# Kernel optimization log

Hardware: AMD Instinct MI355X
Metric: run time of the kernel (lower is better)

## Reference

```python
import jax, jax.numpy as jnp
import numpy as np

B, C, N = 16, 64, 2048
K, KS, OC = 20, 20, 64
BN_EPS = 1e-5


def setup_inputs() -> dict:
    key = jax.random.key(0)
    k1, k2, k3, k4 = jax.random.split(key, 4)
    feature = jax.random.normal(k1, (B, C, N), dtype=jnp.float32)
    neigh_indexs = jax.random.randint(k2, (B * N, K), 0, B * N, dtype=jnp.int64)
    permatrix = jax.random.normal(k3, (B * N, K, KS), dtype=jnp.float32)
    conv_w = jax.random.normal(k4, (OC, 2 * C), dtype=jnp.float32) * 0.05  # 1x1 conv weight
    conv_b = jnp.zeros((OC,), dtype=jnp.float32)
    gamma = jnp.ones((OC,), dtype=jnp.float32)
    beta = jnp.zeros((OC,), dtype=jnp.float32)
    return {"feature": feature, "neigh_indexs": neigh_indexs, "permatrix": permatrix,
            "conv_w": conv_w, "conv_b": conv_b, "gamma": gamma, "beta": beta}


def _forward(feature, neigh_indexs, permatrix, conv_w, conv_b, gamma, beta):
    bsize, num_feat, num_pts = feature.shape
    # [B, C, N] -> [B*N, C]
    flat = jnp.transpose(feature, (0, 2, 1)).reshape(bsize * num_pts, num_feat)
    # neighbor gather: [B*N, K, C] -> [B*N, C, K]
    feats = jnp.transpose(flat[neigh_indexs], (0, 2, 1))
    f_repeat = jnp.broadcast_to(feats[:, :, 0:1], feats.shape)
    f_relative = feats - f_repeat
    feats = jnp.concatenate([f_repeat, f_relative], axis=1)  # [B*N, 2C, K]
    # per-point small matmul with permutation matrix: [B*N, 2C, KS]
    feats = jnp.einsum('nck,nks->ncs', feats, permatrix)
    # 1x1 conv over channel dim: [B*N, OC, KS]
    out = jnp.einsum('ncs,oc->nos', feats, conv_w) + conv_b[None, :, None]
    # max over neighbors, reshape to [B, OC, N]
    out = jnp.max(out, axis=-1).reshape(bsize, num_pts, -1)
    out = jnp.transpose(out, (0, 2, 1))  # [B, OC, N]
    # BatchNorm1d (training-mode forward: biased var over batch & points)
    mean = jnp.mean(out, axis=(0, 2), keepdims=True)
    var = jnp.var(out, axis=(0, 2), keepdims=True)
    out = (out - mean) * jax.lax.rsqrt(var + BN_EPS)
    return out * gamma[None, :, None] + beta[None, :, None]


def reference(feature, neigh_indexs, permatrix, conv_w, conv_b, gamma, beta):
    return _forward(feature, neigh_indexs, permatrix, conv_w, conv_b, gamma, beta)
```

## Files before the change

### kernel.cpp

```cpp
#include <hip/hip_runtime.h>

#define B_   16
#define C_   64
#define N_   2048
#define M_   (B_ * N_)
#define K_   20
#define KS_  20
#define OC_  64
#define NWAVE2 8192
#define NBLK2  2048

__global__ __launch_bounds__(256) void k_project(
    const float* __restrict__ feat,
    const float* __restrict__ conv_w,
    float* __restrict__ pq)
{
    const int lane = threadIdx.x & 63;
    const int wg   = blockIdx.x * 4 + (threadIdx.x >> 6);
    float w2[64], wd[64];
    const float4* cw4 = (const float4*)conv_w;
    #pragma unroll
    for (int j = 0; j < 16; ++j) {
        float4 a = cw4[lane * 32 + j];
        float4 b = cw4[lane * 32 + 16 + j];
        w2[4*j+0] = b.x; w2[4*j+1] = b.y; w2[4*j+2] = b.z; w2[4*j+3] = b.w;
        wd[4*j+0] = a.x - b.x; wd[4*j+1] = a.y - b.y;
        wd[4*j+2] = a.z - b.z; wd[4*j+3] = a.w - b.w;
    }
    const int m0 = wg * 16;
    int b0 = m0 >> 11, p0 = m0 & 2047;
    float fv = feat[((size_t)(b0 * 64 + lane)) * 2048 + p0];
    for (int mi = 0; mi < 16; ++mi) {
        const int m = m0 + mi;
        float fnext = 0.f;
        if (mi < 15) {
            const int mn = m + 1;
            fnext = feat[((size_t)((mn >> 11) * 64 + lane)) * 2048 + (mn & 2047)];
        }
        float p0a = 0.f, p1a = 0.f, q0a = 0.f, q1a = 0.f;
        #pragma unroll
        for (int c = 0; c < 32; ++c) {
            float f0 = __int_as_float(
                __builtin_amdgcn_readlane(__float_as_int(fv), c));
            float f1 = __int_as_float(
                __builtin_amdgcn_readlane(__float_as_int(fv), c + 32));
            p0a = fmaf(w2[c], f0, p0a);
            p1a = fmaf(w2[c + 32], f1, p1a);
            q0a = fmaf(wd[c], f0, q0a);
            q1a = fmaf(wd[c + 32], f1, q1a);
        }
        pq[(size_t)m * 128 + lane]      = p0a + p1a;
        pq[(size_t)m * 128 + 64 + lane] = q0a + q1a;
        fv = fnext;
    }
}

typedef float f16v __attribute__((ext_vector_type(16)));

template<int V, int I>
__device__ __forceinline__ float selv(const f16v& a, const f16v& b,
                                      const f16v& c, const f16v& d,
                                      const f16v& e) {
    if constexpr (V == 0) return a[I];
    else if constexpr (V == 1) return b[I];
    else if constexpr (V == 2) return c[I];
    else if constexpr (V == 3) return d[I];
    else return e[I];
}

template<int KK, bool INIT>
__device__ __forceinline__ void rowfma(float t, float bias, float* acc,
    const f16v& a, const f16v& b, const f16v& c,
    const f16v& d, const f16v& e)
{
    #define RS_(S) { constexpr int e_ = KK * 20 + (S); \
        const float w_ = selv<e_ / 16, e_ % 16>(a, b, c, d, e); \
        acc[S] = fmaf(t, w_, INIT ? bias : acc[S]); }
    RS_(0)  RS_(1)  RS_(2)  RS_(3)  RS_(4)
    RS_(5)  RS_(6)  RS_(7)  RS_(8)  RS_(9)
    RS_(10) RS_(11) RS_(12) RS_(13) RS_(14)
    RS_(15) RS_(16) RS_(17) RS_(18) RS_(19)
    #undef RS_
}

#define CHUNK(CC, INIT0) { \
    f16v sA, sB, sC, sD, sE; \
    asm volatile("s_load_dwordx16 %0, %1, %2" : "=s"(sA) : "s"(psrc), "n"((CC)*320 +   0)); \
    asm volatile("s_load_dwordx16 %0, %1, %2" : "=s"(sB) : "s"(psrc), "n"((CC)*320 +  64)); \
    asm volatile("s_load_dwordx16 %0, %1, %2" : "=s"(sC) : "s"(psrc), "n"((CC)*320 + 128)); \
    asm volatile("s_load_dwordx16 %0, %1, %2" : "=s"(sD) : "s"(psrc), "n"((CC)*320 + 192)); \
    asm volatile("s_load_dwordx16 %0, %1, %2" : "=s"(sE) : "s"(psrc), "n"((CC)*320 + 256)); \
    asm volatile("s_waitcnt lgkmcnt(0)" \
        : "+s"(sA), "+s"(sB), "+s"(sC), "+s"(sD), "+s"(sE)); \
    rowfma<0, INIT0>(pk[(CC)*4+0] + q, bias, acc, sA, sB, sC, sD, sE); \
    rowfma<1, false>(pk[(CC)*4+1] + q, bias, acc, sA, sB, sC, sD, sE); \
    rowfma<2, false>(pk[(CC)*4+2] + q, bias, acc, sA, sB, sC, sD, sE); \
    rowfma<3, false>(pk[(CC)*4+3] + q, bias, acc, sA, sB, sC, sD, sE); }

__global__ __launch_bounds__(256) void k_points(
    const float* __restrict__ pq,
    const int*   __restrict__ nidx,
    const float* __restrict__ perm,
    const float* __restrict__ conv_b,
    float* __restrict__ pre,
    float* __restrict__ partials)
{
    const int tid  = threadIdx.x;
    const int lane = tid & 63;
    const int w    = tid >> 6;
    const int wg   = (int)blockIdx.x * 4 + w;
    const int wgu  = __builtin_amdgcn_readfirstlane(wg);

    const float bias = conv_b[lane];
    float sum = 0.f, sumsq = 0.f;

    int iv = 0;
    if (lane < 20) iv = nidx[(size_t)wg * K_ + lane];

    for (int it = 0; it < 4; ++it) {
        const int n  = wg  + NWAVE2 * it;
        const int nu = wgu + NWAVE2 * it;
        int ik[20];
        #pragma unroll
        for (int k = 0; k < 20; ++k) ik[k] = __builtin_amdgcn_readlane(iv, k);
        float q = pq[(size_t)ik[0] * 128 + 64 + lane];
        float pk[20];
        #pragma unroll
        for (int k = 0; k < 20; ++k) pk[k] = pq[(size_t)ik[k] * 128 + lane];
        if (it < 3) {
            const int nn = n + NWAVE2;
            if (lane < 20) iv = nidx[(size_t)nn * K_ + lane];
        }
        const float* psrc = perm + (size_t)nu * 400;

        float acc[20];
        CHUNK(0, true)
        CHUNK(1, false)
        CHUNK(2, false)
        CHUNK(3, false)
        CHUNK(4, false)

        float mv = acc[0];
        #pragma unroll
        for (int s = 1; s < 20; ++s) mv = fmaxf(mv, acc[s]);
        pre[(size_t)n * 64 + lane] = mv;
        sum += mv;
        sumsq = fmaf(mv, mv, sumsq);
    }

    __shared__ float red[512];
    red[w * 128 + lane]      = sum;
    red[w * 128 + 64 + lane] = sumsq;
    __syncthreads();
    if (tid < 128) {
        float s = red[tid] + red[128 + tid] + red[256 + tid] + red[384 + tid];
        partials[(size_t)blockIdx.x * 128 + tid] = s;
    }
}

#undef CHUNK

__global__ __launch_bounds__(256) void k_stats(
    const float* __restrict__ partials,
    const float* __restrict__ gamma,
    const float* __restrict__ beta,
    float* __restrict__ stats)
{
    const int ch  = blockIdx.x;
    const int tid = threadIdx.x;
    double s = 0.0, s2 = 0.0;
    for (int w = tid; w < NBLK2; w += 256) {
        s  += (double)partials[(size_t)w * 128 + ch];
        s2 += (double)partials[(size_t)w * 128 + 64 + ch];
    }
    __shared__ double sh_s[256];
    __shared__ double sh_q[256];
    sh_s[tid] = s; sh_q[tid] = s2;
    __syncthreads();
    for (int off = 128; off > 0; off >>= 1) {
        if (tid < off) { sh_s[tid] += sh_s[tid + off]; sh_q[tid] += sh_q[tid + off]; }
        __syncthreads();
    }
    if (tid == 0) {
        const double inv_n = 1.0 / (double)M_;
        double mean = sh_s[0] * inv_n;
        double var  = sh_q[0] * inv_n - mean * mean;
        double inv  = 1.0 / sqrt(var + 1e-5);
        double sc   = (double)gamma[ch] * inv;
        stats[ch]      = (float)sc;
        stats[64 + ch] = (float)((double)beta[ch] - mean * sc);
    }
}

__global__ __launch_bounds__(256) void k_apply(
    const float* __restrict__ pre,
    const float* __restrict__ stats,
    float* __restrict__ out)
{
    __shared__ float tile[64 * 65];
    __shared__ float scl[64];
    __shared__ float shf[64];
    const int tid = threadIdx.x;
    if (tid < 64)       scl[tid]      = stats[tid];
    else if (tid < 128) shf[tid - 64] = stats[tid];
    __syncthreads();
    const int b  = blockIdx.x >> 5;
    const int pt = (blockIdx.x & 31) * 64;
    const int c  = tid & 63;
    const int r0 = tid >> 6;
    #pragma unroll
    for (int i = 0; i < 16; ++i) {
        const int r = i * 4 + r0;
        float v = pre[((size_t)(b * 2048 + pt + r)) * 64 + c];
        tile[c * 65 + r] = fmaf(v, scl[c], shf[c]);
    }
    __syncthreads();
    #pragma unroll
    for (int i = 0; i < 16; ++i) {
        const int o = i * 4 + r0;
        out[((size_t)(b * 64 + o)) * 2048 + pt + c] = tile[o * 65 + c];
    }
}

extern "C" void kernel_launch(void* const* d_in, const int* in_sizes, int n_in,
                              void* d_out, int out_size, void* d_ws, size_t ws_size,
                              hipStream_t stream) {
    const float* feat   = (const float*)d_in[0];
    const int*   nidx   = (const int*)  d_in[1];
    const float* perm   = (const float*)d_in[2];
    const float* conv_w = (const float*)d_in[3];
    const float* conv_b = (const float*)d_in[4];
    const float* gamma  = (const float*)d_in[5];
    const float* beta   = (const float*)d_in[6];
    float* out = (float*)d_out;

    char* ws = (char*)d_ws;
    float* pq       = (float*)ws;
    float* pre      = (float*)(ws + (size_t)M_ * 128 * 4);
    float* partials = (float*)(ws + (size_t)M_ * 128 * 4
                                  + (size_t)M_ * 64 * 4);
    float* stats    = (float*)(ws + (size_t)M_ * 128 * 4
                                  + (size_t)M_ * 64 * 4
                                  + (size_t)NBLK2 * 128 * 4);

    hipLaunchKernelGGL(k_project, dim3(512),  dim3(256), 0, stream, feat, conv_w, pq);
    hipLaunchKernelGGL(k_points,  dim3(2048), dim3(256), 0, stream, pq, nidx, perm,
                       conv_b, pre, partials);
    hipLaunchKernelGGL(k_stats,   dim3(64),   dim3(256), 0, stream, partials, gamma,
                       beta, stats);
    hipLaunchKernelGGL(k_apply,   dim3(512),  dim3(256), 0, stream, pre, stats, out);
}
```

Measured before the change: 182.3 us.

## Double-buffer neighbor gathers across point iterations with manual vmcnt waits

The per-point loop in k_points is unrolled into four iterations. The next point's 21 gathered pq loads are issued with inline-asm global_load_dword into a second register buffer before the current point is computed. Explicit s_waitcnt vmcnt counts let gather latency overlap the scalar-perm FMA work, and all four neighbor index vectors are loaded up front. This raises VGPR pressure and relies on hand-counted vmcnt values, so an off-by-one count or a compiler-inserted memory op could cause stale reads.

Measured after the change: 179.0 us. Within noise of the previous version (-1.8%).

```diff
diff --git a/kernel.cpp b/kernel.cpp
--- a/kernel.cpp
+++ b/kernel.cpp
@@ -83,7 +83,7 @@
     #undef RS_
 }
 
-#define CHUNK(CC, INIT0) { \
+#define CHUNK(gar, CC, INIT0) { \
     f16v sA, sB, sC, sD, sE; \
     asm volatile("s_load_dwordx16 %0, %1, %2" : "=s"(sA) : "s"(psrc), "n"((CC)*320 +   0)); \
     asm volatile("s_load_dwordx16 %0, %1, %2" : "=s"(sB) : "s"(psrc), "n"((CC)*320 +  64)); \
@@ -92,10 +92,57 @@
     asm volatile("s_load_dwordx16 %0, %1, %2" : "=s"(sE) : "s"(psrc), "n"((CC)*320 + 256)); \
     asm volatile("s_waitcnt lgkmcnt(0)" \
         : "+s"(sA), "+s"(sB), "+s"(sC), "+s"(sD), "+s"(sE)); \
-    rowfma<0, INIT0>(pk[(CC)*4+0] + q, bias, acc, sA, sB, sC, sD, sE); \
-    rowfma<1, false>(pk[(CC)*4+1] + q, bias, acc, sA, sB, sC, sD, sE); \
-    rowfma<2, false>(pk[(CC)*4+2] + q, bias, acc, sA, sB, sC, sD, sE); \
-    rowfma<3, false>(pk[(CC)*4+3] + q, bias, acc, sA, sB, sC, sD, sE); }
+    rowfma<0, INIT0>(gar[(CC)*4+0] + gar[20], bias, acc, sA, sB, sC, sD, sE); \
+    rowfma<1, false>(gar[(CC)*4+1] + gar[20], bias, acc, sA, sB, sC, sD, sE); \
+    rowfma<2, false>(gar[(CC)*4+2] + gar[20], bias, acc, sA, sB, sC, sD, sE); \
+    rowfma<3, false>(gar[(CC)*4+3] + gar[20], bias, acc, sA, sB, sC, sD, sE); }
+
+__device__ __forceinline__ void issue_gathers(
+    const float* __restrict__ pqt, int ivreg, int voff, float (&g)[21])
+{
+    #pragma unroll
+    for (int k = 0; k < 20; ++k) {
+        const int iku = __builtin_amdgcn_readlane(ivreg, k);
+        const float* sp = pqt + (size_t)(unsigned)iku * 128u;
+        if (k == 0)
+            asm volatile("global_load_dword %0, %1, %2 offset:256"
+                         : "=v"(g[20]) : "v"(voff), "s"(sp));
+        asm volatile("global_load_dword %0, %1, %2"
+                     : "=v"(g[k]) : "v"(voff), "s"(sp));
+    }
+}
+
+#define WAITG(g, CNTTXT) do { \
+    asm volatile("s_waitcnt vmcnt(" CNTTXT ")" : \
+        "+v"(g[0]),"+v"(g[1]),"+v"(g[2]),"+v"(g[3]),"+v"(g[4]), \
+        "+v"(g[5]),"+v"(g[6]),"+v"(g[7]),"+v"(g[8]),"+v"(g[9]), \
+        "+v"(g[10]),"+v"(g[11]),"+v"(g[12]),"+v"(g[13]),"+v"(g[14]), \
+        "+v"(g[15]),"+v"(g[16]),"+v"(g[17]),"+v"(g[18]),"+v"(g[19]), \
+        "+v"(g[20])); \
+    __builtin_amdgcn_sched_barrier(0); \
+} while (0)
+
+#define COMPUTE(gar, NU) { \
+    const float* psrc = perm + (size_t)(NU) * 400; \
+    float acc[20]; \
+    CHUNK(gar, 0, true) \
+    CHUNK(gar, 1, false) \
+    CHUNK(gar, 2, false) \
+    CHUNK(gar, 3, false) \
+    CHUNK(gar, 4, false) \
+    float mv = acc[0]; \
+    mv = fmaxf(mv, acc[1]);  mv = fmaxf(mv, acc[2]);  mv = fmaxf(mv, acc[3]); \
+    mv = fmaxf(mv, acc[4]);  mv = fmaxf(mv, acc[5]);  mv = fmaxf(mv, acc[6]); \
+    mv = fmaxf(mv, acc[7]);  mv = fmaxf(mv, acc[8]);  mv = fmaxf(mv, acc[9]); \
+    mv = fmaxf(mv, acc[10]); mv = fmaxf(mv, acc[11]); mv = fmaxf(mv, acc[12]); \
+    mv = fmaxf(mv, acc[13]); mv = fmaxf(mv, acc[14]); mv = fmaxf(mv, acc[15]); \
+    mv = fmaxf(mv, acc[16]); mv = fmaxf(mv, acc[17]); mv = fmaxf(mv, acc[18]); \
+    mv = fmaxf(mv, acc[19]); \
+    const float* pdst = pre + (size_t)(NU) * 64; \
+    asm volatile("global_store_dword %0, %1, %2" \
+                 :: "v"(voff), "v"(mv), "s"(pdst)); \
+    sum += mv; \
+    sumsq = fmaf(mv, mv, sumsq); }
 
 __global__ __launch_bounds__(256) void k_points(
     const float* __restrict__ pq,
@@ -110,43 +157,35 @@
     const int w    = tid >> 6;
     const int wg   = (int)blockIdx.x * 4 + w;
     const int wgu  = __builtin_amdgcn_readfirstlane(wg);
-
-    const float bias = conv_b[lane];
+    const int voff = lane * 4;
+
+    float bias = conv_b[lane];
     float sum = 0.f, sumsq = 0.f;
 
-    int iv = 0;
-    if (lane < 20) iv = nidx[(size_t)wg * K_ + lane];
-
-    for (int it = 0; it < 4; ++it) {
-        const int n  = wg  + NWAVE2 * it;
-        const int nu = wgu + NWAVE2 * it;
-        int ik[20];
-        #pragma unroll
-        for (int k = 0; k < 20; ++k) ik[k] = __builtin_amdgcn_readlane(iv, k);
-        float q = pq[(size_t)ik[0] * 128 + 64 + lane];
-        float pk[20];
-        #pragma unroll
-        for (int k = 0; k < 20; ++k) pk[k] = pq[(size_t)ik[k] * 128 + lane];
-        if (it < 3) {
-            const int nn = n + NWAVE2;
-            if (lane < 20) iv = nidx[(size_t)nn * K_ + lane];
-        }
-        const float* psrc = perm + (size_t)nu * 400;
-
-        float acc[20];
-        CHUNK(0, true)
-        CHUNK(1, false)
-        CHUNK(2, false)
-        CHUNK(3, false)
-        CHUNK(4, false)
-
-        float mv = acc[0];
-        #pragma unroll
-        for (int s = 1; s < 20; ++s) mv = fmaxf(mv, acc[s]);
-        pre[(size_t)n * 64 + lane] = mv;
-        sum += mv;
-        sumsq = fmaf(mv, mv, sumsq);
-    }
+    int iv0 = 0, iv1 = 0, iv2 = 0, iv3 = 0;
+    if (lane < 20) {
+        iv0 = nidx[(size_t)wgu * K_ + lane];
+        iv1 = nidx[((size_t)wgu +     NWAVE2) * K_ + lane];
+        iv2 = nidx[((size_t)wgu + 2 * NWAVE2) * K_ + lane];
+        iv3 = nidx[((size_t)wgu + 3 * NWAVE2) * K_ + lane];
+    }
+    asm volatile("s_waitcnt vmcnt(0)"
+        : "+v"(bias), "+v"(iv0), "+v"(iv1), "+v"(iv2), "+v"(iv3));
+    __builtin_amdgcn_sched_barrier(0);
+
+    float gA[21], gB[21];
+    issue_gathers(pq, iv0, voff, gA);
+    issue_gathers(pq, iv1, voff, gB);
+    WAITG(gA, "21");
+    COMPUTE(gA, wgu)
+    issue_gathers(pq, iv2, voff, gA);
+    WAITG(gB, "22");
+    COMPUTE(gB, wgu + NWAVE2)
+    issue_gathers(pq, iv3, voff, gB);
+    WAITG(gA, "22");
+    COMPUTE(gA, wgu + 2 * NWAVE2)
+    WAITG(gB, "1");
+    COMPUTE(gB, wgu + 3 * NWAVE2)
 
     __shared__ float red[512];
     red[w * 128 + lane]      = sum;
@@ -158,6 +197,8 @@
     }
 }
 
+#undef COMPUTE
+#undef WAITG
 #undef CHUNK
 
 __global__ __launch_bounds__(256) void k_stats(
```
